# Kernel tuning notes

Measured on AMD Instinct MI355X. Metric: run time of the kernel, lower is better.

## Reference

```python
import jax, jax.numpy as jnp
import numpy as np

D_MODEL = 768
N_HEADS = 12
HEAD_DIM = D_MODEL // N_HEADS
NEG = -10000.0


def setup_inputs() -> dict:
    key = jax.random.key(0)
    ks = jax.random.split(key, 8)
    B, S, D = 2, 2048, D_MODEL
    inp = {
        "q": jax.random.normal(ks[0], (B, S, D), dtype=jnp.float32),
        "k": jax.random.normal(ks[1], (B, S, D), dtype=jnp.float32),
        "v": jax.random.normal(ks[2], (B, S, D), dtype=jnp.float32),
        "attn_mask": jax.random.randint(ks[3], (B, S), 0, 2, dtype=jnp.int32),
        # weights stored [in, out]; apply as x @ W (equivalent to torch Linear)
        "Wq": jax.random.normal(ks[4], (D, D), dtype=jnp.float32) / np.sqrt(D),
        "Wk": jax.random.normal(ks[5], (D, D), dtype=jnp.float32) / np.sqrt(D),
        "Wv": jax.random.normal(ks[6], (D, D), dtype=jnp.float32) / np.sqrt(D),
        "Wo": jax.random.normal(ks[7], (D, D), dtype=jnp.float32) / np.sqrt(D),
        "mask_future": 1,
    }
    return inp


def reference(q, k, v, attn_mask, Wq, Wk, Wv, Wo, mask_future):
    B, S, D = q.shape
    H, hd = N_HEADS, HEAD_DIM
    # project and split heads -> [B, H, S, hd]
    qh = (q @ Wq).reshape(B, S, H, hd).transpose(0, 2, 1, 3)
    kh = (k @ Wk).reshape(B, S, H, hd).transpose(0, 2, 1, 3)
    vh = (v @ Wv).reshape(B, S, H, hd).transpose(0, 2, 1, 3)

    scale = 1.0 / np.sqrt(hd).astype(np.float32)
    # full [B, H, L, S] score matrix (naive SDPA, as in the original)
    scores = jnp.einsum("bhld,bhsd->bhls", qh, kh) * scale
    if mask_future:
        causal = jnp.triu(jnp.full((S, S), NEG, dtype=scores.dtype), k=1)
        scores = scores + causal
    # padding mask: [B, S] -> broadcast over heads and query positions
    pad = attn_mask[:, None, None, :] == 0
    scores = jnp.where(pad, NEG, scores)
    attn = jax.nn.softmax(scores, axis=-1)  # dropout p=0.0 -> identity
    out = jnp.einsum("bhls,bhsd->bhld", attn, vh)  # [B, H, L, hd]
    out = out.transpose(0, 2, 1, 3).reshape(B, S, D)
    return out @ Wo
```

## Files before the change

### kernel.cpp

```cpp
#include <hip/hip_runtime.h>


#define NEGV (-10000.0f)

typedef __attribute__((ext_vector_type(8))) short v8s;
typedef __attribute__((ext_vector_type(4))) float v4f;
typedef __attribute__((ext_vector_type(8))) unsigned short v8u;
typedef __fp16 h2v __attribute__((ext_vector_type(2)));

__device__ __forceinline__ unsigned short f2bf(float f) {
  unsigned int u = __float_as_uint(f);
  u += 0x7FFFu + ((u >> 16) & 1u);
  return (unsigned short)(u >> 16);
}

__device__ __forceinline__ int pkmax_f16(int a, int b) {
  int r;
  asm("v_pk_max_f16 %0, %1, %2" : "=v"(r) : "v"(a), "v"(b));
  return r;
}

__global__ __launch_bounds__(256) void transpose_w(
    const float* __restrict__ w0, const float* __restrict__ w1,
    const float* __restrict__ w2, const float* __restrict__ w3,
    unsigned short* __restrict__ t0, unsigned short* __restrict__ t1,
    unsigned short* __restrict__ t2, unsigned short* __restrict__ t3) {
  const float* w; unsigned short* t;
  switch (blockIdx.z) {
    case 0: w = w0; t = t0; break;
    case 1: w = w1; t = t1; break;
    case 2: w = w2; t = t2; break;
    default: w = w3; t = t3; break;
  }
  __shared__ unsigned short tile[32][33];
  const int tx = threadIdx.x & 31, ty = threadIdx.x >> 5;
  const int x0 = blockIdx.x * 32, y0 = blockIdx.y * 32;
#pragma unroll
  for (int j = 0; j < 4; j++)
    tile[ty + j * 8][tx] = f2bf(w[(size_t)(y0 + ty + j * 8) * 768 + x0 + tx]);
  __syncthreads();
#pragma unroll
  for (int j = 0; j < 4; j++)
    t[(size_t)(x0 + ty + j * 8) * 768 + y0 + tx] = tile[tx][ty + j * 8];
}

__global__ __launch_bounds__(256) void transpose_vh(
    const unsigned short* __restrict__ vh, unsigned short* __restrict__ vht) {
  __shared__ unsigned short tile[32][33];
  const size_t hoff = (size_t)blockIdx.z * 2048 * 64;
  const unsigned short* src = vh + hoff;
  unsigned short* dst = vht + hoff;
  const int s0 = blockIdx.x * 32, d0 = blockIdx.y * 32;
  const int tx = threadIdx.x & 31, ty = threadIdx.x >> 5;
#pragma unroll
  for (int j = 0; j < 4; j++)
    tile[ty + j * 8][tx] = src[(size_t)(s0 + ty + j * 8) * 64 + d0 + tx];
  __syncthreads();
#pragma unroll
  for (int j = 0; j < 4; j++)
    dst[(size_t)(d0 + ty + j * 8) * 2048 + s0 + tx] = tile[tx][ty + j * 8];
}

template <bool ABF16HEAD, bool CF32ROW>
__device__ __forceinline__ void gemm_core(const void* __restrict__ A,
                                          const unsigned short* __restrict__ Wt,
                                          void* __restrict__ C) {
  const int tid = threadIdx.x;
  const int wave = tid >> 6, lane = tid & 63;
  const int quad = lane >> 4, l16 = lane & 15;
  const int wm = wave >> 1, wn = wave & 1;
  const int bm = blockIdx.x * 128, bn = blockIdx.y * 128;

  __shared__ __align__(16) unsigned short As[128 * 32];
  __shared__ __align__(16) unsigned short Bs[128 * 32];

  v4f acc[4][4];
#pragma unroll
  for (int i = 0; i < 4; i++)
#pragma unroll
    for (int j = 0; j < 4; j++) acc[i][j] = (v4f){0.f, 0.f, 0.f, 0.f};

  for (int kt = 0; kt < 24; kt++) {
    __syncthreads();
#pragma unroll
    for (int p = 0; p < 2; p++) {
      int idx = p * 256 + tid;
      int r = idx >> 2, c0 = (idx & 3) << 3;
      int rg = bm + r, c = kt * 32 + c0;
      if (ABF16HEAD) {
        size_t aoff = ((size_t)((rg >> 11) * 12 + (c >> 6)) * 2048 +
                       (rg & 2047)) * 64 + (c & 63);
        *(uint4*)&As[r * 32 + c0] =
            *(const uint4*)((const unsigned short*)A + aoff);
      } else {
        const float* Af = (const float*)A;
        size_t aoff = (size_t)rg * 768 + c;
        float4 x0 = *(const float4*)(Af + aoff);
        float4 x1 = *(const float4*)(Af + aoff + 4);
        v8u tmp;
        tmp[0] = f2bf(x0.x); tmp[1] = f2bf(x0.y);
        tmp[2] = f2bf(x0.z); tmp[3] = f2bf(x0.w);
        tmp[4] = f2bf(x1.x); tmp[5] = f2bf(x1.y);
        tmp[6] = f2bf(x1.z); tmp[7] = f2bf(x1.w);
        *(uint4*)&As[r * 32 + c0] = *(uint4*)&tmp;
      }
      *(uint4*)&Bs[r * 32 + c0] =
          *(const uint4*)&Wt[(size_t)(bn + r) * 768 + c];
    }
    __syncthreads();

    v8s aF[4], bF[4];
#pragma unroll
    for (int mt = 0; mt < 4; mt++)
      aF[mt] = *(const v8s*)&As[(wm * 64 + mt * 16 + l16) * 32 + quad * 8];
#pragma unroll
    for (int nt = 0; nt < 4; nt++)
      bF[nt] = *(const v8s*)&Bs[(wn * 64 + nt * 16 + l16) * 32 + quad * 8];
#pragma unroll
    for (int mt = 0; mt < 4; mt++)
#pragma unroll
      for (int nt = 0; nt < 4; nt++)
        acc[mt][nt] = __builtin_amdgcn_mfma_f32_16x16x32_bf16(
            aF[mt], bF[nt], acc[mt][nt], 0, 0, 0);
  }

#pragma unroll
  for (int mt = 0; mt < 4; mt++) {
#pragma unroll
    for (int i = 0; i < 4; i++) {
      int row = bm + wm * 64 + mt * 16 + quad * 4 + i;
#pragma unroll
      for (int nt = 0; nt < 4; nt++) {
        int col = bn + wn * 64 + nt * 16 + l16;
        if (CF32ROW) {
          ((float*)C)[(size_t)row * 768 + col] = acc[mt][nt][i];
        } else {
          size_t off = ((size_t)((row >> 11) * 12 + (col >> 6)) * 2048 +
                        (row & 2047)) * 64 + (col & 63);
          ((unsigned short*)C)[off] = f2bf(acc[mt][nt][i]);
        }
      }
    }
  }
}

__global__ __launch_bounds__(256) void gemm_qkv(
    const float* __restrict__ xq, const float* __restrict__ xk,
    const float* __restrict__ xv, const unsigned short* __restrict__ wqt,
    const unsigned short* __restrict__ wkt, const unsigned short* __restrict__ wvt,
    unsigned short* __restrict__ qh, unsigned short* __restrict__ kh,
    unsigned short* __restrict__ vh) {
  const float* A; const unsigned short* Wt; unsigned short* C;
  switch (blockIdx.z) {
    case 0: A = xq; Wt = wqt; C = qh; break;
    case 1: A = xk; Wt = wkt; C = kh; break;
    default: A = xv; Wt = wvt; C = vh; break;
  }
  gemm_core<false, false>((const void*)A, Wt, (void*)C);
}

__global__ __launch_bounds__(256) void gemm_o(
    const unsigned short* __restrict__ oat, const unsigned short* __restrict__ wot,
    float* __restrict__ out) {
  gemm_core<true, true>((const void*)oat, wot, (void*)out);
}

__global__ __launch_bounds__(256) void attn_kernel(
    const unsigned short* __restrict__ qh, const unsigned short* __restrict__ kh,
    const unsigned short* __restrict__ vht, const int* __restrict__ attn_mask,
    const int* __restrict__ mask_future, unsigned short* __restrict__ o) {
  const int S = 2048, HD = 64, NH = 12;

  const int nlin = blockIdx.x + 32 * blockIdx.y;
  const int m_ = nlin & 255, t_ = nlin >> 8;
  const int i_ = (t_ == 1) ? (511 - m_) : (t_ * 256 + m_);
  const int qt = 31 - i_ / 24;
  const int bh = i_ - (i_ / 24) * 24;
  const int b = bh / NH, h = bh % NH;

  const int tid = threadIdx.x;
  const int wave = tid >> 6, lane = tid & 63;
  const int quad = lane >> 4, l16 = lane & 15;

  __shared__ __align__(16) unsigned short Ks[64 * 72];
  __shared__ __align__(16) unsigned short Vt[64 * 72];
  __shared__ __align__(16) unsigned short Ps[4][16 * 72];
  __shared__ int Ms[64];
  __shared__ int s_flag;

  const size_t head_off = (size_t)(b * NH + h) * S * HD;
  const unsigned short* Kb = kh + head_off;
  const unsigned short* Vb = vht + head_off;

  const int mf = mask_future[0];
  if (tid == 0) s_flag = 0;

  const int qrowA = qt * 64 + wave * 16 + l16;
  v8s aQ[2];
  {
    const unsigned short* qp = qh + head_off + (size_t)qrowA * HD + quad * 8;
    aQ[0] = *(const v8s*)(qp);
    aQ[1] = *(const v8s*)(qp + 32);
  }
  const int qbase = qt * 64 + wave * 16 + quad * 4;

  float m_i[4];
  v4f accO[4], accL;
#pragma unroll
  for (int i = 0; i < 4; i++) m_i[i] = -1e30f;
  accL = (v4f){0.f, 0.f, 0.f, 0.f};
#pragma unroll
  for (int dt = 0; dt < 4; dt++) accO[dt] = (v4f){0.f, 0.f, 0.f, 0.f};

  v8s ones;
#pragma unroll
  for (int j = 0; j < 8; j++) ones[j] = (short)0x3F80;

  const int kt_causal = mf ? qt : (S / 64 - 1);
  const int r0 = tid >> 3, c0s = (tid & 7) << 3;

  uint4 pk0, pk1, pv0, pv1;
  int pm = 0;
  bool have = false;

  auto prefetch = [&](int kt) {
    const uint4* srck = (const uint4*)(Kb + (size_t)kt * 64 * HD);
    pk0 = srck[tid];
    pk1 = srck[256 + tid];
    const unsigned short* vp = Vb + (size_t)r0 * S + kt * 64 + c0s;
    pv0 = *(const uint4*)vp;
    pv1 = *(const uint4*)(vp + (size_t)32 * S);
    if (tid < 64) pm = attn_mask[b * S + kt * 64 + tid];
  };

  auto stage = [&]() {
    *(uint4*)&Ks[r0 * 72 + c0s] = pk0;
    *(uint4*)&Ks[(r0 + 32) * 72 + c0s] = pk1;
    *(uint4*)&Vt[r0 * 72 + c0s] = pv0;
    *(uint4*)&Vt[(r0 + 32) * 72 + c0s] = pv1;
    if (tid < 64) Ms[tid] = pm;
  };

  for (int phase = 0; phase < 2; phase++) {
    int kt_lo, kt_hi;
    if (phase == 0) { kt_lo = 0; kt_hi = kt_causal; }
    else {
      bool need = (m_i[0] < -5000.f) || (m_i[1] < -5000.f) ||
                  (m_i[2] < -5000.f) || (m_i[3] < -5000.f);
      if (need) s_flag = 1;
      __syncthreads();
      if (!s_flag) break;
      kt_lo = kt_causal + 1; kt_hi = S / 64 - 1;
    }
    for (int kt = kt_lo; kt <= kt_hi; kt++) {
      if (!have) prefetch(kt);
      __syncthreads();
      stage();
      __syncthreads();

      {
        int ktn = -1;
        if (kt < kt_hi) ktn = kt + 1;
        else if (phase == 0 && mf && kt_causal < S / 64 - 1)
          ktn = kt_causal + 1;
        if (ktn >= 0) { prefetch(ktn); have = true; }
        else have = false;
      }

      v4f sc[4];
      __builtin_amdgcn_s_setprio(1);
#pragma unroll
      for (int nt = 0; nt < 4; nt++) {
        const unsigned short* kp = &Ks[(nt * 16 + l16) * 72 + quad * 8];
        v8s b0 = *(const v8s*)kp;
        v8s b1 = *(const v8s*)(kp + 32);
        v4f z = (v4f){0.f, 0.f, 0.f, 0.f};
        z = __builtin_amdgcn_mfma_f32_16x16x32_bf16(aQ[0], b0, z, 0, 0, 0);
        z = __builtin_amdgcn_mfma_f32_16x16x32_bf16(aQ[1], b1, z, 0, 0, 0);
        sc[nt] = z;
      }
      __builtin_amdgcn_s_setprio(0);

#pragma unroll
      for (int nt = 0; nt < 4; nt++) {
        int key = kt * 64 + nt * 16 + l16;
        bool pad = (Ms[nt * 16 + l16] == 0);
#pragma unroll
        for (int i = 0; i < 4; i++) {
          float v = sc[nt][i] * 0.125f;
          v += (mf && (key > qbase + i)) ? NEGV : 0.f;
          v = pad ? NEGV : v;
          sc[nt][i] = v;
        }
      }

      float m4[4];
#pragma unroll
      for (int i = 0; i < 4; i++)
        m4[i] = fmaxf(fmaxf(sc[0][i], sc[1][i]), fmaxf(sc[2][i], sc[3][i]));
      union { h2v h; int v; } pk01, pk23;
      pk01.h = __builtin_amdgcn_cvt_pkrtz(m4[0], m4[1]);
      pk23.h = __builtin_amdgcn_cvt_pkrtz(m4[2], m4[3]);
      int v01 = pk01.v, v23 = pk23.v;
#pragma unroll
      for (int mk = 1; mk <= 8; mk <<= 1) {
        v01 = pkmax_f16(v01, __shfl_xor(v01, mk));
        v23 = pkmax_f16(v23, __shfl_xor(v23, mk));
      }
      union { int v; h2v h; } u01, u23;
      u01.v = v01; u23.v = v23;
      float mx[4] = {(float)u01.h[0], (float)u01.h[1],
                     (float)u23.h[0], (float)u23.h[1]};

#pragma unroll
      for (int i = 0; i < 4; i++) {
        float mnew = fmaxf(m_i[i], mx[i]);
        float alpha = __expf(m_i[i] - mnew);
        m_i[i] = mnew;
#pragma unroll
        for (int nt = 0; nt < 4; nt++)
          sc[nt][i] = __expf(sc[nt][i] - mnew);
#pragma unroll
        for (int dt = 0; dt < 4; dt++) accO[dt][i] *= alpha;
        accL[i] *= alpha;
      }

#pragma unroll
      for (int nt = 0; nt < 4; nt++)
#pragma unroll
        for (int i = 0; i < 4; i++)
          Ps[wave][(quad * 4 + i) * 72 + nt * 16 + l16] = f2bf(sc[nt][i]);

      __builtin_amdgcn_s_setprio(1);
#pragma unroll
      for (int ks = 0; ks < 2; ks++) {
        v8s aP = *(const v8s*)&Ps[wave][l16 * 72 + ks * 32 + quad * 8];
        accL = __builtin_amdgcn_mfma_f32_16x16x32_bf16(aP, ones, accL, 0, 0, 0);
#pragma unroll
        for (int dt = 0; dt < 4; dt++) {
          v8s bV = *(const v8s*)&Vt[(dt * 16 + l16) * 72 + ks * 32 + quad * 8];
          accO[dt] =
              __builtin_amdgcn_mfma_f32_16x16x32_bf16(aP, bV, accO[dt], 0, 0, 0);
        }
      }
      __builtin_amdgcn_s_setprio(0);
    }
    if (phase == 0) __syncthreads();
  }

#pragma unroll
  for (int i = 0; i < 4; i++) {
    float inv = 1.f / accL[i];
    int qr = qbase + i;
    size_t base = head_off + (size_t)qr * HD;
#pragma unroll
    for (int dt = 0; dt < 4; dt++)
      o[base + dt * 16 + l16] = f2bf(accO[dt][i] * inv);
  }
}

extern "C" void kernel_launch(void* const* d_in, const int* in_sizes, int n_in,
                              void* d_out, int out_size, void* d_ws, size_t ws_size,
                              hipStream_t stream) {
  const float* q  = (const float*)d_in[0];
  const float* k  = (const float*)d_in[1];
  const float* v  = (const float*)d_in[2];
  const int* amask = (const int*)d_in[3];
  const float* Wq = (const float*)d_in[4];
  const float* Wk = (const float*)d_in[5];
  const float* Wv = (const float*)d_in[6];
  const float* Wo = (const float*)d_in[7];
  const int* mf  = (const int*)d_in[8];
  float* out = (float*)d_out;

  unsigned short* ws = (unsigned short*)d_ws;
  unsigned short* qh = ws;
  unsigned short* kh = qh + 3145728;
  unsigned short* vh = kh + 3145728;
  unsigned short* wqt = vh + 3145728;
  unsigned short* wkt = wqt + 589824;
  unsigned short* wvt = wkt + 589824;
  unsigned short* wot = wvt + 589824;
  unsigned short* vht = (unsigned short*)d_out;

  transpose_w<<<dim3(24, 24, 4), 256, 0, stream>>>(Wq, Wk, Wv, Wo,
                                                   wqt, wkt, wvt, wot);
  gemm_qkv<<<dim3(32, 6, 3), 256, 0, stream>>>(q, k, v, wqt, wkt, wvt,
                                               qh, kh, vh);
  transpose_vh<<<dim3(64, 2, 24), 256, 0, stream>>>(vh, vht);
  attn_kernel<<<dim3(32, 24), 256, 0, stream>>>(qh, kh, vht, amask, mf, qh);
  gemm_o<<<dim3(32, 6), 256, 0, stream>>>(qh, wot, out);
}
```

Before: 221.5 us.

## Fuse V transpose into QKV GEMM, double-buffer attention K/V tiles, use LDS-direct loads

The V projection now writes its output already transposed (head, dim, seq), which removes the separate transpose_vh kernel launch and its extra memory pass. The attention kernel double-buffers its K, V and mask shared-memory tiles, so one tile is staged while the previous one is consumed, and one of the two barriers per tile is dropped. The GEMM B loads, and the A loads in the output GEMM, use global_load_lds to copy straight into shared memory without passing through registers. The risks are the uncoalesced scattered stores in the transposed V write, doubled LDS use in attention that may lower occupancy, and whether the direct-to-LDS lane layout matches the row-major tile the MFMA reads expect.

```diff
diff --git a/kernel.cpp b/kernel.cpp
--- a/kernel.cpp
+++ b/kernel.cpp
@@ -7,6 +7,11 @@
 typedef __attribute__((ext_vector_type(4))) float v4f;
 typedef __attribute__((ext_vector_type(8))) unsigned short v8u;
 typedef __fp16 h2v __attribute__((ext_vector_type(2)));
+
+#define GLDS16(g, l)                                            \
+  __builtin_amdgcn_global_load_lds(                             \
+      (const __attribute__((address_space(1))) void*)(g),       \
+      (__attribute__((address_space(3))) void*)(l), 16, 0, 0)
 
 __device__ __forceinline__ unsigned short f2bf(float f) {
   unsigned int u = __float_as_uint(f);
@@ -44,24 +49,7 @@
     t[(size_t)(x0 + ty + j * 8) * 768 + y0 + tx] = tile[tx][ty + j * 8];
 }
 
-__global__ __launch_bounds__(256) void transpose_vh(
-    const unsigned short* __restrict__ vh, unsigned short* __restrict__ vht) {
-  __shared__ unsigned short tile[32][33];
-  const size_t hoff = (size_t)blockIdx.z * 2048 * 64;
-  const unsigned short* src = vh + hoff;
-  unsigned short* dst = vht + hoff;
-  const int s0 = blockIdx.x * 32, d0 = blockIdx.y * 32;
-  const int tx = threadIdx.x & 31, ty = threadIdx.x >> 5;
-#pragma unroll
-  for (int j = 0; j < 4; j++)
-    tile[ty + j * 8][tx] = src[(size_t)(s0 + ty + j * 8) * 64 + d0 + tx];
-  __syncthreads();
-#pragma unroll
-  for (int j = 0; j < 4; j++)
-    dst[(size_t)(d0 + ty + j * 8) * 2048 + s0 + tx] = tile[tx][ty + j * 8];
-}
-
-template <bool ABF16HEAD, bool CF32ROW>
+template <bool ABF16HEAD, int CMODE>
 __device__ __forceinline__ void gemm_core(const void* __restrict__ A,
                                           const unsigned short* __restrict__ Wt,
                                           void* __restrict__ C) {
@@ -90,8 +78,8 @@
       if (ABF16HEAD) {
         size_t aoff = ((size_t)((rg >> 11) * 12 + (c >> 6)) * 2048 +
                        (rg & 2047)) * 64 + (c & 63);
-        *(uint4*)&As[r * 32 + c0] =
-            *(const uint4*)((const unsigned short*)A + aoff);
+        GLDS16((const unsigned short*)A + aoff,
+               &As[(size_t)(p * 256 + wave * 64) * 8]);
       } else {
         const float* Af = (const float*)A;
         size_t aoff = (size_t)rg * 768 + c;
@@ -104,8 +92,8 @@
         tmp[6] = f2bf(x1.z); tmp[7] = f2bf(x1.w);
         *(uint4*)&As[r * 32 + c0] = *(uint4*)&tmp;
       }
-      *(uint4*)&Bs[r * 32 + c0] =
-          *(const uint4*)&Wt[(size_t)(bn + r) * 768 + c];
+      GLDS16(&Wt[(size_t)(bn + r) * 768 + c],
+             &Bs[(size_t)(p * 256 + wave * 64) * 8]);
     }
     __syncthreads();
 
@@ -132,11 +120,15 @@
 #pragma unroll
       for (int nt = 0; nt < 4; nt++) {
         int col = bn + wn * 64 + nt * 16 + l16;
-        if (CF32ROW) {
+        if (CMODE == 1) {
           ((float*)C)[(size_t)row * 768 + col] = acc[mt][nt][i];
-        } else {
+        } else if (CMODE == 0) {
           size_t off = ((size_t)((row >> 11) * 12 + (col >> 6)) * 2048 +
                         (row & 2047)) * 64 + (col & 63);
+          ((unsigned short*)C)[off] = f2bf(acc[mt][nt][i]);
+        } else {
+          size_t off = (size_t)((row >> 11) * 12 + (col >> 6)) * (64 * 2048) +
+                       (size_t)(col & 63) * 2048 + (row & 2047);
           ((unsigned short*)C)[off] = f2bf(acc[mt][nt][i]);
         }
       }
@@ -149,20 +141,20 @@
     const float* __restrict__ xv, const unsigned short* __restrict__ wqt,
     const unsigned short* __restrict__ wkt, const unsigned short* __restrict__ wvt,
     unsigned short* __restrict__ qh, unsigned short* __restrict__ kh,
-    unsigned short* __restrict__ vh) {
-  const float* A; const unsigned short* Wt; unsigned short* C;
-  switch (blockIdx.z) {
-    case 0: A = xq; Wt = wqt; C = qh; break;
-    case 1: A = xk; Wt = wkt; C = kh; break;
-    default: A = xv; Wt = wvt; C = vh; break;
-  }
-  gemm_core<false, false>((const void*)A, Wt, (void*)C);
+    unsigned short* __restrict__ vht) {
+  if (blockIdx.z == 2) {
+    gemm_core<false, 2>((const void*)xv, wvt, (void*)vht);
+  } else if (blockIdx.z == 1) {
+    gemm_core<false, 0>((const void*)xk, wkt, (void*)kh);
+  } else {
+    gemm_core<false, 0>((const void*)xq, wqt, (void*)qh);
+  }
 }
 
 __global__ __launch_bounds__(256) void gemm_o(
     const unsigned short* __restrict__ oat, const unsigned short* __restrict__ wot,
     float* __restrict__ out) {
-  gemm_core<true, true>((const void*)oat, wot, (void*)out);
+  gemm_core<true, 1>((const void*)oat, wot, (void*)out);
 }
 
 __global__ __launch_bounds__(256) void attn_kernel(
@@ -182,10 +174,10 @@
   const int wave = tid >> 6, lane = tid & 63;
   const int quad = lane >> 4, l16 = lane & 15;
 
-  __shared__ __align__(16) unsigned short Ks[64 * 72];
-  __shared__ __align__(16) unsigned short Vt[64 * 72];
+  __shared__ __align__(16) unsigned short Ks[2][64 * 72];
+  __shared__ __align__(16) unsigned short Vt[2][64 * 72];
   __shared__ __align__(16) unsigned short Ps[4][16 * 72];
-  __shared__ int Ms[64];
+  __shared__ int Ms[2][64];
   __shared__ int s_flag;
 
   const size_t head_off = (size_t)(b * NH + h) * S * HD;
@@ -219,9 +211,15 @@
   const int kt_causal = mf ? qt : (S / 64 - 1);
   const int r0 = tid >> 3, c0s = (tid & 7) << 3;
 
+  auto nexttile = [&](int t) -> int {
+    if (t < kt_causal) return t + 1;
+    if (t == kt_causal) return (mf && kt_causal < S / 64 - 1) ? t + 1 : -1;
+    return (t < S / 64 - 1) ? t + 1 : -1;
+  };
+
   uint4 pk0, pk1, pv0, pv1;
   int pm = 0;
-  bool have = false;
+  int rtile = -1, stile = -1;
 
   auto prefetch = [&](int kt) {
     const uint4* srck = (const uint4*)(Kb + (size_t)kt * 64 * HD);
@@ -231,14 +229,15 @@
     pv0 = *(const uint4*)vp;
     pv1 = *(const uint4*)(vp + (size_t)32 * S);
     if (tid < 64) pm = attn_mask[b * S + kt * 64 + tid];
+    rtile = kt;
   };
 
-  auto stage = [&]() {
-    *(uint4*)&Ks[r0 * 72 + c0s] = pk0;
-    *(uint4*)&Ks[(r0 + 32) * 72 + c0s] = pk1;
-    *(uint4*)&Vt[r0 * 72 + c0s] = pv0;
-    *(uint4*)&Vt[(r0 + 32) * 72 + c0s] = pv1;
-    if (tid < 64) Ms[tid] = pm;
+  auto stage = [&](int kb) {
+    *(uint4*)&Ks[kb][r0 * 72 + c0s] = pk0;
+    *(uint4*)&Ks[kb][(r0 + 32) * 72 + c0s] = pk1;
+    *(uint4*)&Vt[kb][r0 * 72 + c0s] = pv0;
+    *(uint4*)&Vt[kb][(r0 + 32) * 72 + c0s] = pv1;
+    if (tid < 64) Ms[kb][tid] = pm;
   };
 
   for (int phase = 0; phase < 2; phase++) {
@@ -251,27 +250,38 @@
       __syncthreads();
       if (!s_flag) break;
       kt_lo = kt_causal + 1; kt_hi = S / 64 - 1;
+      if (kt_lo > kt_hi) break;
     }
+
+    if (stile != kt_lo) {
+      if (rtile != kt_lo) prefetch(kt_lo);
+      stage(kt_lo & 1);
+      stile = kt_lo;
+      int nx = nexttile(kt_lo);
+      if (nx >= 0) prefetch(nx);
+    }
+
     for (int kt = kt_lo; kt <= kt_hi; kt++) {
-      if (!have) prefetch(kt);
       __syncthreads();
-      stage();
-      __syncthreads();
-
-      {
-        int ktn = -1;
-        if (kt < kt_hi) ktn = kt + 1;
-        else if (phase == 0 && mf && kt_causal < S / 64 - 1)
-          ktn = kt_causal + 1;
-        if (ktn >= 0) { prefetch(ktn); have = true; }
-        else have = false;
-      }
+
+      int nkt = nexttile(kt);
+      if (nkt >= 0 && stile != nkt) {
+        stage(nkt & 1);
+        stile = nkt;
+        int n2 = nexttile(nkt);
+        if (n2 >= 0) prefetch(n2);
+      }
+
+      const int kb = kt & 1;
+      const unsigned short* KsB = Ks[kb];
+      const unsigned short* VtB = Vt[kb];
+      const int* MsB = Ms[kb];
 
       v4f sc[4];
       __builtin_amdgcn_s_setprio(1);
 #pragma unroll
       for (int nt = 0; nt < 4; nt++) {
-        const unsigned short* kp = &Ks[(nt * 16 + l16) * 72 + quad * 8];
+        const unsigned short* kp = &KsB[(nt * 16 + l16) * 72 + quad * 8];
         v8s b0 = *(const v8s*)kp;
         v8s b1 = *(const v8s*)(kp + 32);
         v4f z = (v4f){0.f, 0.f, 0.f, 0.f};
@@ -284,7 +294,7 @@
 #pragma unroll
       for (int nt = 0; nt < 4; nt++) {
         int key = kt * 64 + nt * 16 + l16;
-        bool pad = (Ms[nt * 16 + l16] == 0);
+        bool pad = (MsB[nt * 16 + l16] == 0);
 #pragma unroll
         for (int i = 0; i < 4; i++) {
           float v = sc[nt][i] * 0.125f;
@@ -338,7 +348,7 @@
         accL = __builtin_amdgcn_mfma_f32_16x16x32_bf16(aP, ones, accL, 0, 0, 0);
 #pragma unroll
         for (int dt = 0; dt < 4; dt++) {
-          v8s bV = *(const v8s*)&Vt[(dt * 16 + l16) * 72 + ks * 32 + quad * 8];
+          v8s bV = *(const v8s*)&VtB[(dt * 16 + l16) * 72 + ks * 32 + quad * 8];
           accO[dt] =
               __builtin_amdgcn_mfma_f32_16x16x32_bf16(aP, bV, accO[dt], 0, 0, 0);
         }
@@ -386,8 +396,7 @@
   transpose_w<<<dim3(24, 24, 4), 256, 0, stream>>>(Wq, Wk, Wv, Wo,
                                                    wqt, wkt, wvt, wot);
   gemm_qkv<<<dim3(32, 6, 3), 256, 0, stream>>>(q, k, v, wqt, wkt, wvt,
-                                               qh, kh, vh);
-  transpose_vh<<<dim3(64, 2, 24), 256, 0, stream>>>(vh, vht);
+                                               qh, kh, vht);
   attn_kernel<<<dim3(32, 24), 256, 0, stream>>>(qh, kh, vht, amask, mf, qh);
   gemm_o<<<dim3(32, 6), 256, 0, stream>>>(qh, wot, out);
 }
```

Result: slower. 237.3 us (+7.1%).
